# Performance work log

Measured on AMD Instinct MI355X. Metric: run time of the kernel, lower is better.

The kernel has to match this reference:

```python
import jax, jax.numpy as jnp
import numpy as np
from jax import lax

B, T, L, H, K, NL, NB = 32, 512, 2048, 512, 3, 2, 256
PAD = (K - 1) // 2
EPS = 1e-5


def _predictor_params(key):
    k1, k2 = jax.random.split(key)
    s = 1.0 / np.sqrt(H * K).astype(np.float32)
    return dict(
        conv_w=jax.random.normal(k1, (NL, H, H, K), jnp.float32) * s,
        conv_b=jnp.zeros((NL, H), jnp.float32),
        ln_g=jnp.ones((NL, H), jnp.float32),
        ln_b=jnp.zeros((NL, H), jnp.float32),
        lin_w=jax.random.normal(k2, (H, 1), jnp.float32) * 0.02,
        lin_b=jnp.zeros((1,), jnp.float32),
    )


def setup_inputs():
    key = jax.random.key(0)
    ks = jax.random.split(key, 8)
    inp = {
        'x': jax.random.normal(ks[0], (B, T, H), jnp.float32),
        'src_mask': jnp.zeros((B, T), bool),
        'duration_target': jax.random.randint(ks[1], (B, T), 0, 8, jnp.int32),
        'pitch_target': jax.random.normal(ks[2], (B, T), jnp.float32),
        'energy_target': jax.random.uniform(ks[3], (B, T), jnp.float32),
        'max_len': L,
    }
    for name, k in zip(('dur', 'pit', 'en'), ks[4:7]):
        for p, v in _predictor_params(k).items():
            inp[name + '_' + p] = v
    inp['pitch_bins'] = jnp.linspace(-3.0, 3.0, NB - 1)
    inp['energy_bins'] = jnp.linspace(0.0, 1.0, NB - 1)
    k1, k2 = jax.random.split(ks[7])
    inp['pitch_emb'] = jax.random.normal(k1, (NB, H), jnp.float32) * 0.02
    inp['energy_emb'] = jax.random.normal(k2, (NB, H), jnp.float32) * 0.02
    return inp


def _layer_norm(h, g, b):
    m = jnp.mean(h, -1, keepdims=True)
    v = jnp.var(h, -1, keepdims=True)
    return (h - m) * lax.rsqrt(v + EPS) * g + b


def _predictor(x, cw, cb, lg, lb, lw, lbias, mask):
    # stack of [Conv1d(k=3,same) -> ReLU -> LayerNorm] x NL, then Linear -> 1
    out = x
    for i in range(NL):
        h = lax.conv_general_dilated(out.transpose(0, 2, 1), cw[i], (1,), [(PAD, PAD)],
                                     dimension_numbers=('NCH', 'OIH', 'NCH'))
        h = h.transpose(0, 2, 1) + cb[i]  # [B, T, H]
        out = _layer_norm(jax.nn.relu(h), lg[i], lb[i])
    out = (out @ lw)[..., 0] + lbias[0]  # [B, T]
    return jnp.where(mask, 0.0, out)


def _length_regulate(x, duration, max_len):
    # vectorized equivalent of the per-token expand+concat+pad loop
    csum = jnp.cumsum(duration, axis=1)                     # [B, T]
    frames = jnp.arange(max_len)                            # [L]
    idx = jax.vmap(lambda c: jnp.searchsorted(c, frames, side='right'))(csum)  # [B, L]
    idx = jnp.clip(idx, 0, x.shape[1] - 1)
    out = jnp.take_along_axis(x, idx[:, :, None], axis=1)   # [B, L, H]
    mel_len = jnp.minimum(csum[:, -1], max_len)             # [B]
    out = out * (frames[None, :] < mel_len[:, None])[..., None]
    return out, mel_len


def reference(x, src_mask, duration_target, pitch_target, energy_target, max_len,
              dur_conv_w, dur_conv_b, dur_ln_g, dur_ln_b, dur_lin_w, dur_lin_b,
              pit_conv_w, pit_conv_b, pit_ln_g, pit_ln_b, pit_lin_w, pit_lin_b,
              en_conv_w, en_conv_b, en_ln_g, en_ln_b, en_lin_w, en_lin_b,
              pitch_bins, energy_bins, pitch_emb, energy_emb):
    log_d = _predictor(x, dur_conv_w, dur_conv_b, dur_ln_g, dur_ln_b, dur_lin_w, dur_lin_b, src_mask)
    pitch_pred = _predictor(x, pit_conv_w, pit_conv_b, pit_ln_g, pit_ln_b, pit_lin_w, pit_lin_b, src_mask)
    energy_pred = _predictor(x, en_conv_w, en_conv_b, en_ln_g, en_ln_b, en_lin_w, en_lin_b, src_mask)
    # torch.bucketize(target, bins) (right=False) == searchsorted side='left'
    p_emb = pitch_emb[jnp.searchsorted(pitch_bins, pitch_target, side='left')]
    e_emb = energy_emb[jnp.searchsorted(energy_bins, energy_target, side='left')]
    x2 = x + p_emb + e_emb
    out, mel_len = _length_regulate(x2, duration_target, max_len)
    return (out, pitch_pred, energy_pred, log_d, mel_len)
```

## Files before the change

kernel.cpp:

```cpp
#include <hip/hip_runtime.h>
#include <hip/hip_bf16.h>

#define B_ 32
#define T_ 512
#define TP_ 514
#define L_ 2048
#define H_ 512
#define NRR (B_*T_)
#define KC_ 1536
#define NB_ 256
#define EPS_ 1e-5f
#define XPE ((size_t)B_ * TP_ * H_)

typedef __bf16 bf16;
typedef __bf16 bf16x8 __attribute__((ext_vector_type(8)));
typedef float f32x4 __attribute__((ext_vector_type(4)));

static const size_t WC_BYTES  = (size_t)6 * H_ * KC_ * 2;
static const size_t XP_BYTES  = XPE * 2;
static const size_t Y_BYTES   = (size_t)3 * NRR * H_ * 2;

__device__ __forceinline__ void gload16(const void* g, void* l) {
    __builtin_amdgcn_global_load_lds(
        (const __attribute__((address_space(1))) unsigned int*)g,
        (__attribute__((address_space(3))) unsigned int*)l, 16, 0, 0);
}

__global__ void k_prep_wc(const float* __restrict__ wd, const float* __restrict__ wp,
                          const float* __restrict__ we, bf16* __restrict__ wc) {
    int e = blockIdx.x * 256 + threadIdx.x;
    if (e >= 6 * H_ * KC_) return;
    int m   = e / (H_ * KC_);
    int rem = e % (H_ * KC_);
    int o  = rem / KC_;
    int r2 = rem % KC_;
    int k  = r2 / H_;
    int c  = r2 % H_;
    int p = m >> 1, i = m & 1;
    const float* w = (p == 0) ? wd : (p == 1 ? wp : we);
    float v = w[((size_t)i * H_ * H_ + (size_t)o * H_ + c) * 3 + k];
    wc[e] = (bf16)v;
}

__global__ void k_pad(const float* __restrict__ x, bf16* __restrict__ xp0,
                      bf16* __restrict__ xp1) {
    int wid = threadIdx.x >> 6, lane = threadIdx.x & 63;
    int row = blockIdx.x * 4 + wid;
    int b = row / TP_, tp = row % TP_;
    bf16* d0 = xp0 + (size_t)row * H_ + lane * 8;
    if (tp == 0 || tp == TP_ - 1) {
        bf16x8 z;
#pragma unroll
        for (int i = 0; i < 8; ++i) z[i] = (bf16)0.0f;
        *(bf16x8*)d0 = z;
#pragma unroll
        for (int p = 0; p < 3; ++p)
            *(bf16x8*)(xp1 + p * XPE + (size_t)row * H_ + lane * 8) = z;
    } else {
        const f32x4* p = (const f32x4*)(x + ((size_t)(b * T_ + tp - 1)) * H_ + lane * 8);
        f32x4 u = p[0], v = p[1];
        bf16x8 o;
        o[0] = (bf16)u[0]; o[1] = (bf16)u[1]; o[2] = (bf16)u[2]; o[3] = (bf16)u[3];
        o[4] = (bf16)v[0]; o[5] = (bf16)v[1]; o[6] = (bf16)v[2]; o[7] = (bf16)v[3];
        *(bf16x8*)d0 = o;
    }
}

__global__ void k_scan(const int* __restrict__ dur, int* __restrict__ csum,
                       float* __restrict__ mel_out) {
    int b = blockIdx.x, t = threadIdx.x;
    __shared__ int s[T_];
    s[t] = dur[b * T_ + t];
    __syncthreads();
    for (int off = 1; off < T_; off <<= 1) {
        int v = (t >= off) ? s[t - off] : 0;
        __syncthreads();
        s[t] += v;
        __syncthreads();
    }
    csum[b * T_ + t] = s[t];
    if (t == T_ - 1) mel_out[b] = (float)((s[t] < L_) ? s[t] : L_);
}

__global__ void k_gather(const float* __restrict__ x, const float* __restrict__ pemb,
                         const float* __restrict__ eemb, const float* __restrict__ pt,
                         const float* __restrict__ et, const float* __restrict__ pbins,
                         const float* __restrict__ ebins, const int* __restrict__ csum,
                         float* __restrict__ out) {
    int bi = blockIdx.x;
    int b  = bi >> 5;
    int lbase = (bi & 31) * 64;
    __shared__ int cs[T_];
    __shared__ float pb[NB_ - 1], eb[NB_ - 1];
    cs[threadIdx.x]       = csum[b * T_ + threadIdx.x];
    cs[threadIdx.x + 256] = csum[b * T_ + threadIdx.x + 256];
    if (threadIdx.x < NB_ - 1) {
        pb[threadIdx.x] = pbins[threadIdx.x];
        eb[threadIdx.x] = ebins[threadIdx.x];
    }
    __syncthreads();
    int wid = threadIdx.x >> 6, lane = threadIdx.x & 63;
    int mel = cs[T_ - 1]; if (mel > L_) mel = L_;
#pragma unroll 1
    for (int it = 0; it < 16; ++it) {
        int l = lbase + it * 4 + wid;
        float* op = out + ((size_t)(b * L_ + l)) * H_ + lane * 8;
        if (l >= mel) {
            f32x4 z = {0.f, 0.f, 0.f, 0.f};
            ((f32x4*)op)[0] = z;
            ((f32x4*)op)[1] = z;
            continue;
        }
        int lo = 0, hi = T_;
        while (lo < hi) { int mid = (lo + hi) >> 1; if (cs[mid] <= l) lo = mid + 1; else hi = mid; }
        int idx = (lo < T_ - 1) ? lo : (T_ - 1);
        int rr = b * T_ + idx;
        float pv = pt[rr], ev = et[rr];
        int pi, ei;
        { int a = 0, c = NB_ - 1; while (a < c) { int mid = (a + c) >> 1; if (pb[mid] < pv) a = mid + 1; else c = mid; } pi = a; }
        { int a = 0, c = NB_ - 1; while (a < c) { int mid = (a + c) >> 1; if (eb[mid] < ev) a = mid + 1; else c = mid; } ei = a; }
        const f32x4* xp = (const f32x4*)(x    + (size_t)rr * H_ + lane * 8);
        const f32x4* pp = (const f32x4*)(pemb + (size_t)pi * H_ + lane * 8);
        const f32x4* ep = (const f32x4*)(eemb + (size_t)ei * H_ + lane * 8);
        ((f32x4*)op)[0] = xp[0] + pp[0] + ep[0];
        ((f32x4*)op)[1] = xp[1] + pp[1] + ep[1];
    }
}

template<int LAYER>
__global__ __launch_bounds__(256)
void k_gemm(const bf16* __restrict__ Xp, const bf16* __restrict__ Wall,
            const float* __restrict__ cb0, const float* __restrict__ cb1,
            const float* __restrict__ cb2, bf16* __restrict__ Y) {
    __shared__ bf16 lA[136 * 64];
    __shared__ bf16 lB[3 * 128 * 64];

    int bid = blockIdx.x;
    int xcd = bid & 7, idx = bid >> 3;
    int colblk = idx >> 4;
    int rowblk = xcd * 16 + (idx & 15);
    int p  = colblk >> 2;
    int oB = (colblk & 3) * 128;
    int rowBase = rowblk * 128;

    const bf16* A = (LAYER == 0) ? Xp : (Xp + (size_t)p * XPE);
    const bf16* W = Wall + ((size_t)(2 * p + LAYER) * H_ + oB) * KC_;
    const float* cbp  = (p == 0) ? cb0 : (p == 1 ? cb1 : cb2);
    const float* bias = cbp + LAYER * H_;

    int tid = threadIdx.x;
    int wid = tid >> 6, lane = tid & 63;
    int wm = wid >> 1, wn = wid & 1;
    int lr = lane & 15, kq = lane >> 4;
    int rsub = lane >> 3;
    int csw  = ((lane & 7) ^ rsub) << 3;
    int b = rowBase >> 9, t0 = rowBase & (T_ - 1);
    const bf16* Abase = A + ((size_t)(b * TP_ + t0)) * H_;

    f32x4 acc[4][4];
#pragma unroll
    for (int m = 0; m < 4; ++m)
#pragma unroll
        for (int n = 0; n < 4; ++n) acc[m][n] = (f32x4){0.f, 0.f, 0.f, 0.f};

    for (int s = 0; s < 8; ++s) {
        int c0 = s * 64;
#pragma unroll
        for (int q = 0; q < 5; ++q) {
            int g = q * 4 + wid;
            if (g < 17)
                gload16(Abase + (size_t)(g * 8 + rsub) * H_ + c0 + csw, &lA[g * 8 * 64]);
        }
#pragma unroll
        for (int tap = 0; tap < 3; ++tap)
#pragma unroll
            for (int q = 0; q < 4; ++q) {
                int g = q * 4 + wid;
                gload16(W + (size_t)(g * 8 + rsub) * KC_ + tap * H_ + c0 + csw,
                        &lB[(tap * 128 + g * 8) * 64]);
            }
        __syncthreads();

#pragma unroll
        for (int tap = 0; tap < 3; ++tap) {
            bf16x8 af[4][2], bfr[4][2];
            int ka = (lr + tap) & 7, kb = lr & 7;
#pragma unroll
            for (int m = 0; m < 4; ++m)
#pragma unroll
                for (int kk = 0; kk < 2; ++kk)
                    af[m][kk] = *(const bf16x8*)&lA[(wm * 64 + m * 16 + lr + tap) * 64 +
                                                    ((((kk * 4 + kq) ^ ka)) << 3)];
#pragma unroll
            for (int n = 0; n < 4; ++n)
#pragma unroll
                for (int kk = 0; kk < 2; ++kk)
                    bfr[n][kk] = *(const bf16x8*)&lB[(tap * 128 + wn * 64 + n * 16 + lr) * 64 +
                                                     ((((kk * 4 + kq) ^ kb)) << 3)];
#pragma unroll
            for (int m = 0; m < 4; ++m)
#pragma unroll
                for (int n = 0; n < 4; ++n)
#pragma unroll
                    for (int kk = 0; kk < 2; ++kk)
                        acc[m][n] = __builtin_amdgcn_mfma_f32_16x16x32_bf16(
                            af[m][kk], bfr[n][kk], acc[m][n], 0, 0, 0);
        }
        __syncthreads();
    }

#pragma unroll
    for (int n = 0; n < 4; ++n) {
        int o = oB + wn * 64 + n * 16 + lr;
        float bi = bias[o];
#pragma unroll
        for (int m = 0; m < 4; ++m) {
            int row = rowBase + wm * 64 + m * 16 + 4 * kq;
#pragma unroll
            for (int r = 0; r < 4; ++r)
                Y[((size_t)p * NRR + row + r) * H_ + o] = (bf16)fmaxf(acc[m][n][r] + bi, 0.f);
        }
    }
}

__global__ void k_ln_store(const bf16* __restrict__ Yin,
                           const float* __restrict__ g0, const float* __restrict__ g1,
                           const float* __restrict__ g2,
                           const float* __restrict__ bb0, const float* __restrict__ bb1,
                           const float* __restrict__ bb2, bf16* __restrict__ xp1) {
    int wid = threadIdx.x >> 6, lane = threadIdx.x & 63;
    int rg = blockIdx.x * 4 + wid;
    int p = rg >> 14, r = rg & (NRR - 1);
    const float* g   = (p == 0) ? g0 : (p == 1 ? g1 : g2);
    const float* bta = (p == 0) ? bb0 : (p == 1 ? bb1 : bb2);
    bf16x8 a = *(const bf16x8*)(Yin + ((size_t)p * NRR + r) * H_ + lane * 8);
    float f[8];
#pragma unroll
    for (int i = 0; i < 8; ++i) f[i] = (float)a[i];
    float s1 = 0.f, s2 = 0.f;
#pragma unroll
    for (int i = 0; i < 8; ++i) { s1 += f[i]; s2 += f[i] * f[i]; }
    for (int m = 1; m < 64; m <<= 1) { s1 += __shfl_xor(s1, m); s2 += __shfl_xor(s2, m); }
    float mean = s1 * (1.f / H_);
    float var  = s2 * (1.f / H_) - mean * mean;
    float rs   = rsqrtf(var + EPS_);
    const f32x4* gp = (const f32x4*)g;
    const f32x4* bp = (const f32x4*)bta;
    f32x4 ga = gp[lane * 2], gb = gp[lane * 2 + 1];
    f32x4 ba = bp[lane * 2], bbv = bp[lane * 2 + 1];
    bf16x8 o;
    o[0] = (bf16)((f[0] - mean) * rs * ga[0] + ba[0]);
    o[1] = (bf16)((f[1] - mean) * rs * ga[1] + ba[1]);
    o[2] = (bf16)((f[2] - mean) * rs * ga[2] + ba[2]);
    o[3] = (bf16)((f[3] - mean) * rs * ga[3] + ba[3]);
    o[4] = (bf16)((f[4] - mean) * rs * gb[0] + bbv[0]);
    o[5] = (bf16)((f[5] - mean) * rs * gb[1] + bbv[1]);
    o[6] = (bf16)((f[6] - mean) * rs * gb[2] + bbv[2]);
    o[7] = (bf16)((f[7] - mean) * rs * gb[3] + bbv[3]);
    int bb = r >> 9, t = r & (T_ - 1);
    *(bf16x8*)(xp1 + (size_t)p * XPE + ((size_t)(bb * TP_ + t + 1)) * H_ + lane * 8) = o;
}

__global__ void k_ln_linear(const bf16* __restrict__ Yin,
                            const float* __restrict__ g0, const float* __restrict__ g1,
                            const float* __restrict__ g2,
                            const float* __restrict__ bb0, const float* __restrict__ bb1,
                            const float* __restrict__ bb2,
                            const float* __restrict__ w0p, const float* __restrict__ w1p,
                            const float* __restrict__ w2p,
                            const float* __restrict__ lb0, const float* __restrict__ lb1,
                            const float* __restrict__ lb2,
                            const unsigned char* __restrict__ mask,
                            float* __restrict__ o0, float* __restrict__ o1,
                            float* __restrict__ o2) {
    int wid = threadIdx.x >> 6, lane = threadIdx.x & 63;
    int rg = blockIdx.x * 4 + wid;
    int p = rg >> 14, r = rg & (NRR - 1);
    const float* g   = ((p == 0) ? g0 : (p == 1 ? g1 : g2)) + H_;
    const float* bta = ((p == 0) ? bb0 : (p == 1 ? bb1 : bb2)) + H_;
    const float* lw  = (p == 0) ? w0p : (p == 1 ? w1p : w2p);
    const float* lb  = (p == 0) ? lb0 : (p == 1 ? lb1 : lb2);
    float*       op  = (p == 0) ? o0 : (p == 1 ? o1 : o2);
    bf16x8 a = *(const bf16x8*)(Yin + ((size_t)p * NRR + r) * H_ + lane * 8);
    float f[8];
#pragma unroll
    for (int i = 0; i < 8; ++i) f[i] = (float)a[i];
    float s1 = 0.f, s2 = 0.f;
#pragma unroll
    for (int i = 0; i < 8; ++i) { s1 += f[i]; s2 += f[i] * f[i]; }
    for (int m = 1; m < 64; m <<= 1) { s1 += __shfl_xor(s1, m); s2 += __shfl_xor(s2, m); }
    float mean = s1 * (1.f / H_);
    float var  = s2 * (1.f / H_) - mean * mean;
    float rs   = rsqrtf(var + EPS_);
    const f32x4* gp = (const f32x4*)g;
    const f32x4* bp = (const f32x4*)bta;
    const f32x4* wp = (const f32x4*)lw;
    f32x4 ga = gp[lane * 2], gb = gp[lane * 2 + 1];
    f32x4 ba = bp[lane * 2], bbv = bp[lane * 2 + 1];
    f32x4 wa = wp[lane * 2], wb = wp[lane * 2 + 1];
    float s = ((f[0] - mean) * rs * ga[0] + ba[0]) * wa[0]
            + ((f[1] - mean) * rs * ga[1] + ba[1]) * wa[1]
            + ((f[2] - mean) * rs * ga[2] + ba[2]) * wa[2]
            + ((f[3] - mean) * rs * ga[3] + ba[3]) * wa[3]
            + ((f[4] - mean) * rs * gb[0] + bbv[0]) * wb[0]
            + ((f[5] - mean) * rs * gb[1] + bbv[1]) * wb[1]
            + ((f[6] - mean) * rs * gb[2] + bbv[2]) * wb[2]
            + ((f[7] - mean) * rs * gb[3] + bbv[3]) * wb[3];
    for (int m = 1; m < 64; m <<= 1) s += __shfl_xor(s, m);
    if (lane == 0) op[r] = mask[r] ? 0.f : (s + lb[0]);
}

extern "C" void kernel_launch(void* const* d_in, const int* in_sizes, int n_in,
                              void* d_out, int out_size, void* d_ws, size_t ws_size,
                              hipStream_t stream) {
    const float* x  = (const float*)d_in[0];
    const unsigned char* mask = (const unsigned char*)d_in[1];
    const int*   dur = (const int*)d_in[2];
    const float* pt  = (const float*)d_in[3];
    const float* et  = (const float*)d_in[4];
    const float* cw[3]    = {(const float*)d_in[6],  (const float*)d_in[12], (const float*)d_in[18]};
    const float* cb[3]    = {(const float*)d_in[7],  (const float*)d_in[13], (const float*)d_in[19]};
    const float* lg[3]    = {(const float*)d_in[8],  (const float*)d_in[14], (const float*)d_in[20]};
    const float* lbn[3]   = {(const float*)d_in[9],  (const float*)d_in[15], (const float*)d_in[21]};
    const float* lw[3]    = {(const float*)d_in[10], (const float*)d_in[16], (const float*)d_in[22]};
    const float* lbias[3] = {(const float*)d_in[11], (const float*)d_in[17], (const float*)d_in[23]};
    const float* pbins = (const float*)d_in[24];
    const float* ebins = (const float*)d_in[25];
    const float* pemb  = (const float*)d_in[26];
    const float* eemb  = (const float*)d_in[27];

    float* out0 = (float*)d_out;
    const size_t OUT0 = (size_t)B_ * L_ * H_;
    float* pitch_out  = out0 + OUT0;
    float* energy_out = pitch_out + NRR;
    float* logd_out   = energy_out + NRR;
    float* mel_out    = logd_out + NRR;

    char* ws = (char*)d_ws;
    bf16*  wc   = (bf16*)ws;
    bf16*  xp0  = (bf16*)(ws + WC_BYTES);
    bf16*  xp1  = (bf16*)(ws + WC_BYTES + XP_BYTES);
    bf16*  y    = (bf16*)(ws + WC_BYTES + 4 * XP_BYTES);
    int*   csum = (int*)(ws + WC_BYTES + 4 * XP_BYTES + Y_BYTES);

    k_prep_wc<<<(6 * H_ * KC_ + 255) / 256, 256, 0, stream>>>(cw[0], cw[1], cw[2], wc);
    k_pad<<<B_ * TP_ / 4, 256, 0, stream>>>(x, xp0, xp1);
    k_scan<<<B_, T_, 0, stream>>>(dur, csum, mel_out);
    k_gather<<<B_ * 32, 256, 0, stream>>>(x, pemb, eemb, pt, et, pbins, ebins, csum, out0);

    k_gemm<0><<<1536, 256, 0, stream>>>(xp0, wc, cb[0], cb[1], cb[2], y);
    k_ln_store<<<3 * NRR / 4, 256, 0, stream>>>(y, lg[0], lg[1], lg[2],
                                                lbn[0], lbn[1], lbn[2], xp1);
    k_gemm<1><<<1536, 256, 0, stream>>>(xp1, wc, cb[0], cb[1], cb[2], y);
    k_ln_linear<<<3 * NRR / 4, 256, 0, stream>>>(y, lg[0], lg[1], lg[2],
                                                 lbn[0], lbn[1], lbn[2],
                                                 lw[0], lw[1], lw[2],
                                                 lbias[0], lbias[1], lbias[2],
                                                 mask, logd_out, pitch_out, energy_out);
}
```

Before: 248.8 us.

## Enlarge conv GEMM row tile to 256 with 32-wide K slices

The conv-as-GEMM kernel now computes 256 rows by 128 output channels per block instead of 128x128, with each warp holding 8x4 accumulators. The K step shrinks from 64 to 32 so LDS stays similar, and the swizzle and load mapping are reworked for 32-element rows. Larger tiles raise MFMA work per loaded byte and halve the grid to 768 blocks. In exchange, register pressure rises, fewer blocks fit per CU, and there are twice as many K iterations with barriers.

```diff
diff --git a/kernel.cpp b/kernel.cpp
--- a/kernel.cpp
+++ b/kernel.cpp
@@ -132,16 +132,16 @@
 void k_gemm(const bf16* __restrict__ Xp, const bf16* __restrict__ Wall,
             const float* __restrict__ cb0, const float* __restrict__ cb1,
             const float* __restrict__ cb2, bf16* __restrict__ Y) {
-    __shared__ bf16 lA[136 * 64];
-    __shared__ bf16 lB[3 * 128 * 64];
+    __shared__ bf16 lA[272 * 32];
+    __shared__ bf16 lB[384 * 32];
 
     int bid = blockIdx.x;
     int xcd = bid & 7, idx = bid >> 3;
-    int colblk = idx >> 4;
-    int rowblk = xcd * 16 + (idx & 15);
+    int colblk = idx >> 3;
+    int rowblk = xcd * 8 + (idx & 7);
     int p  = colblk >> 2;
     int oB = (colblk & 3) * 128;
-    int rowBase = rowblk * 128;
+    int rowBase = rowblk * 256;
 
     const bf16* A = (LAYER == 0) ? Xp : (Xp + (size_t)p * XPE);
     const bf16* W = Wall + ((size_t)(2 * p + LAYER) * H_ + oB) * KC_;
@@ -152,59 +152,53 @@
     int wid = tid >> 6, lane = tid & 63;
     int wm = wid >> 1, wn = wid & 1;
     int lr = lane & 15, kq = lane >> 4;
-    int rsub = lane >> 3;
-    int csw  = ((lane & 7) ^ rsub) << 3;
+    int srow = lane >> 2;
+    int csw  = (((lane & 3) ^ ((lane >> 3) & 3)) << 3);
     int b = rowBase >> 9, t0 = rowBase & (T_ - 1);
     const bf16* Abase = A + ((size_t)(b * TP_ + t0)) * H_;
 
-    f32x4 acc[4][4];
-#pragma unroll
-    for (int m = 0; m < 4; ++m)
+    f32x4 acc[8][4];
+#pragma unroll
+    for (int m = 0; m < 8; ++m)
 #pragma unroll
         for (int n = 0; n < 4; ++n) acc[m][n] = (f32x4){0.f, 0.f, 0.f, 0.f};
 
-    for (int s = 0; s < 8; ++s) {
-        int c0 = s * 64;
+    for (int s = 0; s < 16; ++s) {
+        int c0 = s * 32;
 #pragma unroll
         for (int q = 0; q < 5; ++q) {
             int g = q * 4 + wid;
             if (g < 17)
-                gload16(Abase + (size_t)(g * 8 + rsub) * H_ + c0 + csw, &lA[g * 8 * 64]);
-        }
-#pragma unroll
-        for (int tap = 0; tap < 3; ++tap)
-#pragma unroll
-            for (int q = 0; q < 4; ++q) {
-                int g = q * 4 + wid;
-                gload16(W + (size_t)(g * 8 + rsub) * KC_ + tap * H_ + c0 + csw,
-                        &lB[(tap * 128 + g * 8) * 64]);
+                gload16(Abase + (size_t)(g * 16 + srow) * H_ + c0 + csw, &lA[g * 16 * 32]);
+        }
+#pragma unroll
+        for (int q = 0; q < 6; ++q) {
+            int g = q * 4 + wid;
+            int tap = g >> 3;
+            int o = ((g & 7) * 16) + srow;
+            gload16(W + (size_t)o * KC_ + tap * H_ + c0 + csw, &lB[g * 16 * 32]);
+        }
+        __syncthreads();
+
+#pragma unroll
+        for (int tap = 0; tap < 3; ++tap) {
+            bf16x8 af[8], bfr[4];
+#pragma unroll
+            for (int n = 0; n < 4; ++n) {
+                int row = tap * 128 + wn * 64 + n * 16 + lr;
+                bfr[n] = *(const bf16x8*)&lB[row * 32 + ((kq ^ ((row >> 1) & 3)) << 3)];
             }
-        __syncthreads();
-
-#pragma unroll
-        for (int tap = 0; tap < 3; ++tap) {
-            bf16x8 af[4][2], bfr[4][2];
-            int ka = (lr + tap) & 7, kb = lr & 7;
-#pragma unroll
-            for (int m = 0; m < 4; ++m)
-#pragma unroll
-                for (int kk = 0; kk < 2; ++kk)
-                    af[m][kk] = *(const bf16x8*)&lA[(wm * 64 + m * 16 + lr + tap) * 64 +
-                                                    ((((kk * 4 + kq) ^ ka)) << 3)];
-#pragma unroll
-            for (int n = 0; n < 4; ++n)
-#pragma unroll
-                for (int kk = 0; kk < 2; ++kk)
-                    bfr[n][kk] = *(const bf16x8*)&lB[(tap * 128 + wn * 64 + n * 16 + lr) * 64 +
-                                                     ((((kk * 4 + kq) ^ kb)) << 3)];
-#pragma unroll
-            for (int m = 0; m < 4; ++m)
+#pragma unroll
+            for (int m = 0; m < 8; ++m) {
+                int row = wm * 128 + m * 16 + lr + tap;
+                af[m] = *(const bf16x8*)&lA[row * 32 + ((kq ^ ((row >> 1) & 3)) << 3)];
+            }
+#pragma unroll
+            for (int m = 0; m < 8; ++m)
 #pragma unroll
                 for (int n = 0; n < 4; ++n)
-#pragma unroll
-                    for (int kk = 0; kk < 2; ++kk)
-                        acc[m][n] = __builtin_amdgcn_mfma_f32_16x16x32_bf16(
-                            af[m][kk], bfr[n][kk], acc[m][n], 0, 0, 0);
+                    acc[m][n] = __builtin_amdgcn_mfma_f32_16x16x32_bf16(
+                        af[m], bfr[n], acc[m][n], 0, 0, 0);
         }
         __syncthreads();
     }
@@ -214,8 +208,8 @@
         int o = oB + wn * 64 + n * 16 + lr;
         float bi = bias[o];
 #pragma unroll
-        for (int m = 0; m < 4; ++m) {
-            int row = rowBase + wm * 64 + m * 16 + 4 * kq;
+        for (int m = 0; m < 8; ++m) {
+            int row = rowBase + wm * 128 + m * 16 + 4 * kq;
 #pragma unroll
             for (int r = 0; r < 4; ++r)
                 Y[((size_t)p * NRR + row + r) * H_ + o] = (bf16)fmaxf(acc[m][n][r] + bi, 0.f);
@@ -348,10 +342,10 @@
     k_scan<<<B_, T_, 0, stream>>>(dur, csum, mel_out);
     k_gather<<<B_ * 32, 256, 0, stream>>>(x, pemb, eemb, pt, et, pbins, ebins, csum, out0);
 
-    k_gemm<0><<<1536, 256, 0, stream>>>(xp0, wc, cb[0], cb[1], cb[2], y);
+    k_gemm<0><<<768, 256, 0, stream>>>(xp0, wc, cb[0], cb[1], cb[2], y);
     k_ln_store<<<3 * NRR / 4, 256, 0, stream>>>(y, lg[0], lg[1], lg[2],
                                                 lbn[0], lbn[1], lbn[2], xp1);
-    k_gemm<1><<<1536, 256, 0, stream>>>(xp1, wc, cb[0], cb[1], cb[2], y);
+    k_gemm<1><<<768, 256, 0, stream>>>(xp1, wc, cb[0], cb[1], cb[2], y);
     k_ln_linear<<<3 * NRR / 4, 256, 0, stream>>>(y, lg[0], lg[1], lg[2],
                                                  lbn[0], lbn[1], lbn[2],
                                                  lw[0], lw[1], lw[2],
```

Result: slower. 307.8 us (+23.7%).
